# Kernel optimization log

Hardware: AMD Instinct MI355X
Metric: run time of the kernel (lower is better)

Reference implementation:

```python
import jax, jax.numpy as jnp
import numpy as np

ANG = 5  # angRes; n = ANG*ANG
EPS = 1e-12  # torch F.normalize eps

def _l2norm(x, axis):
    n = jnp.sqrt(jnp.sum(x * x, axis=axis, keepdims=True))
    return x / jnp.maximum(n, EPS)

def setup_inputs() -> dict:
    key = jax.random.key(0)
    kq, kk, kv = jax.random.split(key, 3)
    shape = (16, 16, 25, 16, 128)  # b c n h w
    return {
        "token_q": jax.random.normal(kq, shape, dtype=jnp.float32),
        "token_k": jax.random.normal(kk, shape, dtype=jnp.float32),
        "token_v": jax.random.normal(kv, shape, dtype=jnp.float32),
    }

def reference(token_q, token_k, token_v):
    b, c, n, h, w = token_q.shape
    u = v = ANG
    buffer = token_v

    def to_q(x):  # b c (u v) h w -> b (c h) (w u v)
        return x.reshape(b, c, u, v, h, w).transpose(0, 1, 4, 5, 2, 3).reshape(b, c * h, w * u * v)

    def to_k(x):  # b c (u v) h w -> b (w u v) (c h)
        return x.reshape(b, c, u, v, h, w).transpose(0, 5, 2, 3, 1, 4).reshape(b, w * u * v, c * h)

    unfold_q = _l2norm(to_q(token_q), axis=-1)      # [b, ch, wuv]
    unfold_k = _l2norm(to_k(token_k), axis=-2)      # [b, wuv, ch]
    unfold_v = to_q(token_v)                        # [b, ch, wuv]

    att = jnp.einsum('bts,bsr->btr', unfold_q, unfold_k)  # [b, ch, ch]
    size = c * h
    causal = jnp.tril(jnp.ones((size, size), dtype=bool))
    att = jnp.where(causal, att, jnp.float32(-1e15))
    att = jax.nn.softmax(att, axis=-1)

    out = jnp.einsum('btr,brs->bts', att, unfold_v)  # [b, ch, wuv]
    # b (c h) (w u v) -> b c (u v) h w
    out = out.reshape(b, c, h, w, u, v).transpose(0, 1, 4, 5, 2, 3).reshape(b, c, n, h, w)
    return out + buffer
```

## Files before the change

### kernel.cpp

```cpp
#include <hip/hip_runtime.h>
#include <math.h>

#define SB 819200
#define SC 51200
#define SN 2048
#define CH 256
#define NW 3200
#define NPARTS 5
#define PARTLEN 640
#define SPART 1048576
#define G1BLOCKS 240

typedef __bf16 bf16x8 __attribute__((ext_vector_type(8)));
typedef __bf16 bf16x4 __attribute__((ext_vector_type(4)));
typedef __bf16 bf16x2 __attribute__((ext_vector_type(2)));
typedef float  f32x4  __attribute__((ext_vector_type(4)));

__device__ __forceinline__ bf16x8 cvt8(float4 a, float4 b) {
    bf16x8 r;
    r[0] = (__bf16)a.x; r[1] = (__bf16)a.y; r[2] = (__bf16)a.z; r[3] = (__bf16)a.w;
    r[4] = (__bf16)b.x; r[5] = (__bf16)b.y; r[6] = (__bf16)b.z; r[7] = (__bf16)b.w;
    return r;
}

__global__ __launch_bounds__(256, 2) void gemm1_norms_kernel(const float* __restrict__ q,
                                                             const float* __restrict__ k,
                                                             float* __restrict__ Sp,
                                                             float* __restrict__ inv_nq,
                                                             float* __restrict__ inv_nk) {
    __shared__ alignas(16) __bf16 As[128 * 72];
    __shared__ alignas(16) __bf16 Bs[128 * 72];

    const int tid = threadIdx.x;
    const int lane = tid & 63;
    const int wave = tid >> 6;

    if (blockIdx.x >= G1BLOCKS) {
        const int row = (blockIdx.x - G1BLOCKS) * 4 + wave;
        const int b = row >> 8;
        const int t = row & 255;
        const size_t base = (size_t)b * SB + (size_t)(t >> 4) * SC +
                            (size_t)(t & 15) * 128 + lane * 2;
        float sq = 0.f, sk = 0.f;
#pragma unroll
        for (int nch = 0; nch < 25; nch++) {
            const float2 a = *(const float2*)(q + base + (size_t)nch * SN);
            const float2 c = *(const float2*)(k + base + (size_t)nch * SN);
            sq += a.x * a.x + a.y * a.y;
            sk += c.x * c.x + c.y * c.y;
        }
#pragma unroll
        for (int off = 32; off; off >>= 1) {
            sq += __shfl_xor(sq, off, 64);
            sk += __shfl_xor(sk, off, 64);
        }
        if (lane == 0) {
            inv_nq[row] = 1.0f / fmaxf(sqrtf(sq), 1e-12f);
            inv_nk[row] = 1.0f / fmaxf(sqrtf(sk), 1e-12f);
        }
        return;
    }

    const int bx = blockIdx.x;
    const int tile = bx % 3;
    const int part = (bx / 3) % NPARTS;
    const int b = bx / (3 * NPARTS);
    const int tm = (tile + 1) >> 1;
    const int tn = tile >> 1;

    const int wm = wave >> 1;
    const int wn = wave & 1;

    const int srow = tid >> 1;
    const int scol = (tid & 1) * 32;
    const int ta = tm * 128 + srow;
    const int rb = tn * 128 + srow;
    const float* qrow = q + (size_t)b * SB + (size_t)(ta >> 4) * SC + (size_t)(ta & 15) * 128;
    const float* krow = k + (size_t)b * SB + (size_t)(rb >> 4) * SC + (size_t)(rb & 15) * 128;

    f32x4 acc[4][4] = {};
    bool live[4][4];
#pragma unroll
    for (int mi = 0; mi < 4; mi++)
#pragma unroll
        for (int ni = 0; ni < 4; ni++)
            live[mi][ni] = (tn * 128 + wn * 64 + ni * 16) <= (tm * 128 + wm * 64 + mi * 16);

    for (int ch = 0; ch < 10; ch++) {
        const int kg = part * PARTLEN + ch * 64;
        const size_t koff = (size_t)(kg >> 7) * SN + (kg & 127) + scol;

        float4 av[8], bv[8];
#pragma unroll
        for (int j = 0; j < 8; j++) {
            av[j] = *(const float4*)(qrow + koff + j * 4);
            bv[j] = *(const float4*)(krow + koff + j * 4);
        }
        __syncthreads();
#pragma unroll
        for (int j = 0; j < 4; j++) {
            *(bf16x8*)&As[srow * 72 + scol + j * 8] = cvt8(av[2 * j], av[2 * j + 1]);
            *(bf16x8*)&Bs[srow * 72 + scol + j * 8] = cvt8(bv[2 * j], bv[2 * j + 1]);
        }
        __syncthreads();
#pragma unroll
        for (int ks = 0; ks < 2; ks++) {
            const int ko = ks * 32 + (lane >> 4) * 8;
            bf16x8 af[4], bf[4];
#pragma unroll
            for (int mi = 0; mi < 4; mi++)
                af[mi] = *(const bf16x8*)&As[(wm * 64 + mi * 16 + (lane & 15)) * 72 + ko];
#pragma unroll
            for (int ni = 0; ni < 4; ni++)
                bf[ni] = *(const bf16x8*)&Bs[(wn * 64 + ni * 16 + (lane & 15)) * 72 + ko];
#pragma unroll
            for (int mi = 0; mi < 4; mi++)
#pragma unroll
                for (int ni = 0; ni < 4; ni++)
                    if (live[mi][ni])
                        acc[mi][ni] = __builtin_amdgcn_mfma_f32_16x16x32_bf16(
                            af[mi], bf[ni], acc[mi][ni], 0, 0, 0);
        }
    }

    float* o = Sp + (size_t)part * SPART + (size_t)b * 65536;
#pragma unroll
    for (int mi = 0; mi < 4; mi++)
#pragma unroll
        for (int ni = 0; ni < 4; ni++) {
            if (!live[mi][ni]) continue;
            const int r = tn * 128 + wn * 64 + ni * 16 + (lane & 15);
#pragma unroll
            for (int j = 0; j < 4; j++) {
                const int t = tm * 128 + wm * 64 + mi * 16 + (lane >> 4) * 4 + j;
                o[(size_t)t * 256 + r] = acc[mi][ni][j];
            }
        }
}

__global__ __launch_bounds__(256) void softmax_kernel(const float* __restrict__ Sp,
                                                      const float* __restrict__ inv_nq,
                                                      const float* __restrict__ inv_nk,
                                                      __bf16* __restrict__ P) {
    const int wave = threadIdx.x >> 6;
    const int lane = threadIdx.x & 63;
    const int t = blockIdx.x * 4 + wave;
    const int b = blockIdx.y;
    const size_t rowbase = ((size_t)b * 256 + t) * 256;
    const int r0 = lane * 4;

    float4 s4 = {0.f, 0.f, 0.f, 0.f};
#pragma unroll
    for (int p = 0; p < NPARTS; p++) {
        const float4 x = *(const float4*)(Sp + (size_t)p * SPART + rowbase + r0);
        s4.x += x.x; s4.y += x.y; s4.z += x.z; s4.w += x.w;
    }
    const float qn = inv_nq[b * 256 + t];
    const float4 kn = *(const float4*)(inv_nk + b * 256 + r0);

    float val[4] = {s4.x * qn * kn.x, s4.y * qn * kn.y,
                    s4.z * qn * kn.z, s4.w * qn * kn.w};
    float m = -1e30f;
#pragma unroll
    for (int j = 0; j < 4; j++) {
        if (r0 + j > t) val[j] = -1e30f;
        m = fmaxf(m, val[j]);
    }
#pragma unroll
    for (int off = 32; off; off >>= 1) m = fmaxf(m, __shfl_xor(m, off, 64));

    float e[4], sum = 0.f;
#pragma unroll
    for (int j = 0; j < 4; j++) {
        e[j] = (r0 + j <= t) ? expf(val[j] - m) : 0.f;
        sum += e[j];
    }
#pragma unroll
    for (int off = 32; off; off >>= 1) sum += __shfl_xor(sum, off, 64);

    const float inv = 1.0f / sum;
    bf16x4 o;
    o[0] = (__bf16)(e[0] * inv);
    o[1] = (__bf16)(e[1] * inv);
    o[2] = (__bf16)(e[2] * inv);
    o[3] = (__bf16)(e[3] * inv);
    *(bf16x4*)(P + rowbase + r0) = o;
}

__global__ __launch_bounds__(256, 4) void gemm2_kernel(const __bf16* __restrict__ P,
                                                       const float* __restrict__ v,
                                                       float* __restrict__ out) {
    __shared__ alignas(16) char smem[9216];
    __bf16* Vs = (__bf16*)smem;
    float* Es = (float*)smem;

    const int tid = threadIdx.x;
    const int b = blockIdx.z;
    const int tt = blockIdx.y;
    const int nw = blockIdx.x;
    const int n = nw >> 1;
    const int whalf = nw & 1;

    const int lane = tid & 63;
    const int wave = tid >> 6;
    const int wm = wave >> 1;
    const int wn = wave & 1;
    const int l15 = lane & 15;
    const int quad = lane >> 4;

    const int vu = tid & 7;
    const int rp = tid >> 3;
    const float* vbase = v + (size_t)b * SB + (size_t)n * SN + whalf * 64;

    const __bf16* Pbase = P + ((size_t)b * 256 + tt * 128 + wm * 64 + l15) * 256 + quad * 8;

    f32x4 acc[4][2] = {};

    for (int kc = 0; kc < 4; kc++) {
        bf16x8 af[4][2];
#pragma unroll
        for (int mi = 0; mi < 4; mi++)
#pragma unroll
            for (int ks = 0; ks < 2; ks++)
                af[mi][ks] = *(const bf16x8*)(Pbase + (size_t)mi * 16 * 256 + kc * 64 + ks * 32);

        float vr0[8], vr1[8];
        {
            const int r0 = kc * 64 + 2 * rp;
            const int r1 = r0 + 1;
            const float* row0 = vbase + (size_t)(r0 >> 4) * SC + (size_t)(r0 & 15) * 128;
            const float* row1 = vbase + (size_t)(r1 >> 4) * SC + (size_t)(r1 & 15) * 128;
            *(float4*)&vr0[0] = *(const float4*)(row0 + vu * 8);
            *(float4*)&vr0[4] = *(const float4*)(row0 + vu * 8 + 4);
            *(float4*)&vr1[0] = *(const float4*)(row1 + vu * 8);
            *(float4*)&vr1[4] = *(const float4*)(row1 + vu * 8 + 4);
        }
        __syncthreads();
        {
            const int rl0 = 2 * rp;
#pragma unroll
            for (int sj = 0; sj < 8; sj++) {
                const int s = vu * 8 + sj;
                bf16x2 pr;
                pr[0] = (__bf16)vr0[sj];
                pr[1] = (__bf16)vr1[sj];
                *(bf16x2*)&Vs[s * 72 + (rl0 ^ (s & 0x38))] = pr;
            }
        }
        __syncthreads();
#pragma unroll
        for (int ks = 0; ks < 2; ks++) {
            bf16x8 bfr[2];
#pragma unroll
            for (int ni = 0; ni < 2; ni++) {
                const int s = wn * 32 + ni * 16 + l15;
                bfr[ni] = *(const bf16x8*)&Vs[s * 72 + ((ks * 32 + quad * 8) ^ (s & 0x38))];
            }
#pragma unroll
            for (int mi = 0; mi < 4; mi++)
#pragma unroll
                for (int ni = 0; ni < 2; ni++)
                    acc[mi][ni] = __builtin_amdgcn_mfma_f32_16x16x32_bf16(
                        af[mi][ks], bfr[ni], acc[mi][ni], 0, 0, 0);
        }
    }

    for (int p = 0; p < 4; p++) {
        __syncthreads();
        if (wm == (p >> 1)) {
            const int mibase = (p & 1) * 2;
#pragma unroll
            for (int mm = 0; mm < 2; mm++)
#pragma unroll
                for (int ni = 0; ni < 2; ni++) {
                    const f32x4 a = acc[mibase + mm][ni];
                    const int wcol = wn * 32 + ni * 16 + l15;
#pragma unroll
                    for (int j = 0; j < 4; j++)
                        Es[(mm * 16 + quad * 4 + j) * 68 + wcol] = a[j];
                }
        }
        __syncthreads();
#pragma unroll
        for (int it = 0; it < 2; it++) {
            const int tl = it * 16 + (tid >> 4);
            const int w4 = (tid & 15) * 4;
            const int t = tt * 128 + p * 32 + tl;
            const size_t a = (size_t)b * SB + (size_t)(t >> 4) * SC + (size_t)n * SN +
                             (size_t)(t & 15) * 128 + whalf * 64 + w4;
            float4 r4 = *(const float4*)&Es[tl * 68 + w4];
            const float4 buf = *(const float4*)(v + a);
            r4.x += buf.x; r4.y += buf.y; r4.z += buf.z; r4.w += buf.w;
            *(float4*)(out + a) = r4;
        }
    }
}

extern "C" void kernel_launch(void* const* d_in, const int* in_sizes, int n_in,
                              void* d_out, int out_size, void* d_ws, size_t ws_size,
                              hipStream_t stream) {
    const float* q = (const float*)d_in[0];
    const float* k = (const float*)d_in[1];
    const float* v = (const float*)d_in[2];
    float* out = (float*)d_out;

    float* ws = (float*)d_ws;
    float* inv_nq = ws;
    float* inv_nk = ws + 4096;
    __bf16* P = (__bf16*)(ws + 8192);

    float* Spart = out;

    gemm1_norms_kernel<<<dim3(G1BLOCKS + 1024), dim3(256), 0, stream>>>(
        q, k, Spart, inv_nq, inv_nk);
    softmax_kernel<<<dim3(64, 16), dim3(256), 0, stream>>>(Spart, inv_nq, inv_nk, P);
    gemm2_kernel<<<dim3(50, 2, 16), dim3(256), 0, stream>>>(P, v, out);
}
```

Measured before the change: 228.4 us.

## Fuse norm computation into gemm1, double-split K, and prefetch next chunk

Removes the separate norm blocks by accumulating squared row norms from the q/k tiles already loaded in gemm1. Partial norms are written per K-part and reduced in the softmax kernel. K is split into 10 parts instead of 5 to double the gemm1 grid. Global loads for the next chunk are issued before the MFMA work on the current one to overlap latency. This trades extra partial-sum traffic in softmax and workspace for fewer redundant q/k reads.

```diff
diff --git a/kernel.cpp b/kernel.cpp
--- a/kernel.cpp
+++ b/kernel.cpp
@@ -6,10 +6,11 @@
 #define SN 2048
 #define CH 256
 #define NW 3200
-#define NPARTS 5
-#define PARTLEN 640
+#define NPARTS 10
+#define PARTLEN 320
+#define NCHUNK 5
 #define SPART 1048576
-#define G1BLOCKS 240
+#define G1BLOCKS 480
 
 typedef __bf16 bf16x8 __attribute__((ext_vector_type(8)));
 typedef __bf16 bf16x4 __attribute__((ext_vector_type(4)));
@@ -23,43 +24,21 @@
     return r;
 }
 
-__global__ __launch_bounds__(256, 2) void gemm1_norms_kernel(const float* __restrict__ q,
-                                                             const float* __restrict__ k,
-                                                             float* __restrict__ Sp,
-                                                             float* __restrict__ inv_nq,
-                                                             float* __restrict__ inv_nk) {
+__device__ __forceinline__ float dot4(float4 a) {
+    return a.x * a.x + a.y * a.y + a.z * a.z + a.w * a.w;
+}
+
+__global__ __launch_bounds__(256, 2) void gemm1_kernel(const float* __restrict__ q,
+                                                       const float* __restrict__ k,
+                                                       float* __restrict__ Sp,
+                                                       float* __restrict__ nq2p,
+                                                       float* __restrict__ nk2p) {
     __shared__ alignas(16) __bf16 As[128 * 72];
     __shared__ alignas(16) __bf16 Bs[128 * 72];
 
     const int tid = threadIdx.x;
     const int lane = tid & 63;
     const int wave = tid >> 6;
-
-    if (blockIdx.x >= G1BLOCKS) {
-        const int row = (blockIdx.x - G1BLOCKS) * 4 + wave;
-        const int b = row >> 8;
-        const int t = row & 255;
-        const size_t base = (size_t)b * SB + (size_t)(t >> 4) * SC +
-                            (size_t)(t & 15) * 128 + lane * 2;
-        float sq = 0.f, sk = 0.f;
-#pragma unroll
-        for (int nch = 0; nch < 25; nch++) {
-            const float2 a = *(const float2*)(q + base + (size_t)nch * SN);
-            const float2 c = *(const float2*)(k + base + (size_t)nch * SN);
-            sq += a.x * a.x + a.y * a.y;
-            sk += c.x * c.x + c.y * c.y;
-        }
-#pragma unroll
-        for (int off = 32; off; off >>= 1) {
-            sq += __shfl_xor(sq, off, 64);
-            sk += __shfl_xor(sk, off, 64);
-        }
-        if (lane == 0) {
-            inv_nq[row] = 1.0f / fmaxf(sqrtf(sq), 1e-12f);
-            inv_nk[row] = 1.0f / fmaxf(sqrtf(sk), 1e-12f);
-        }
-        return;
-    }
 
     const int bx = blockIdx.x;
     const int tile = bx % 3;
@@ -78,6 +57,9 @@
     const float* qrow = q + (size_t)b * SB + (size_t)(ta >> 4) * SC + (size_t)(ta & 15) * 128;
     const float* krow = k + (size_t)b * SB + (size_t)(rb >> 4) * SC + (size_t)(rb & 15) * 128;
 
+    const bool doQ = (tile != 2);
+    const bool doK = (tile != 1);
+
     f32x4 acc[4][4] = {};
     bool live[4][4];
 #pragma unroll
@@ -86,23 +68,43 @@
         for (int ni = 0; ni < 4; ni++)
             live[mi][ni] = (tn * 128 + wn * 64 + ni * 16) <= (tm * 128 + wm * 64 + mi * 16);
 
-    for (int ch = 0; ch < 10; ch++) {
-        const int kg = part * PARTLEN + ch * 64;
+    float sqa = 0.f, sqb = 0.f;
+    float4 av[8], bv[8];
+
+    {
+        const int kg = part * PARTLEN;
         const size_t koff = (size_t)(kg >> 7) * SN + (kg & 127) + scol;
-
-        float4 av[8], bv[8];
 #pragma unroll
         for (int j = 0; j < 8; j++) {
             av[j] = *(const float4*)(qrow + koff + j * 4);
             bv[j] = *(const float4*)(krow + koff + j * 4);
         }
-        __syncthreads();
 #pragma unroll
         for (int j = 0; j < 4; j++) {
             *(bf16x8*)&As[srow * 72 + scol + j * 8] = cvt8(av[2 * j], av[2 * j + 1]);
             *(bf16x8*)&Bs[srow * 72 + scol + j * 8] = cvt8(bv[2 * j], bv[2 * j + 1]);
         }
-        __syncthreads();
+        if (doQ) {
+#pragma unroll
+            for (int j = 0; j < 8; j++) sqa += dot4(av[j]);
+        }
+        if (doK) {
+#pragma unroll
+            for (int j = 0; j < 8; j++) sqb += dot4(bv[j]);
+        }
+    }
+    __syncthreads();
+
+    for (int ch = 0; ch < NCHUNK; ch++) {
+        if (ch < NCHUNK - 1) {
+            const int kg = part * PARTLEN + (ch + 1) * 64;
+            const size_t koff = (size_t)(kg >> 7) * SN + (kg & 127) + scol;
+#pragma unroll
+            for (int j = 0; j < 8; j++) {
+                av[j] = *(const float4*)(qrow + koff + j * 4);
+                bv[j] = *(const float4*)(krow + koff + j * 4);
+            }
+        }
 #pragma unroll
         for (int ks = 0; ks < 2; ks++) {
             const int ko = ks * 32 + (lane >> 4) * 8;
@@ -121,6 +123,23 @@
                         acc[mi][ni] = __builtin_amdgcn_mfma_f32_16x16x32_bf16(
                             af[mi], bf[ni], acc[mi][ni], 0, 0, 0);
         }
+        if (ch < NCHUNK - 1) {
+            __syncthreads();
+#pragma unroll
+            for (int j = 0; j < 4; j++) {
+                *(bf16x8*)&As[srow * 72 + scol + j * 8] = cvt8(av[2 * j], av[2 * j + 1]);
+                *(bf16x8*)&Bs[srow * 72 + scol + j * 8] = cvt8(bv[2 * j], bv[2 * j + 1]);
+            }
+            if (doQ) {
+#pragma unroll
+                for (int j = 0; j < 8; j++) sqa += dot4(av[j]);
+            }
+            if (doK) {
+#pragma unroll
+                for (int j = 0; j < 8; j++) sqb += dot4(bv[j]);
+            }
+            __syncthreads();
+        }
     }
 
     float* o = Sp + (size_t)part * SPART + (size_t)b * 65536;
@@ -136,11 +155,18 @@
                 o[(size_t)t * 256 + r] = acc[mi][ni][j];
             }
         }
+
+    sqa += __shfl_xor(sqa, 1, 64);
+    sqb += __shfl_xor(sqb, 1, 64);
+    if (!(lane & 1)) {
+        if (doQ) nq2p[part * 4096 + b * 256 + ta] = sqa;
+        if (doK) nk2p[part * 4096 + b * 256 + rb] = sqb;
+    }
 }
 
 __global__ __launch_bounds__(256) void softmax_kernel(const float* __restrict__ Sp,
-                                                      const float* __restrict__ inv_nq,
-                                                      const float* __restrict__ inv_nk,
+                                                      const float* __restrict__ nq2p,
+                                                      const float* __restrict__ nk2p,
                                                       __bf16* __restrict__ P) {
     const int wave = threadIdx.x >> 6;
     const int lane = threadIdx.x & 63;
@@ -155,8 +181,21 @@
         const float4 x = *(const float4*)(Sp + (size_t)p * SPART + rowbase + r0);
         s4.x += x.x; s4.y += x.y; s4.z += x.z; s4.w += x.w;
     }
-    const float qn = inv_nq[b * 256 + t];
-    const float4 kn = *(const float4*)(inv_nk + b * 256 + r0);
+    float sq = 0.f;
+#pragma unroll
+    for (int p = 0; p < NPARTS; p++) sq += nq2p[p * 4096 + b * 256 + t];
+    float4 sk = {0.f, 0.f, 0.f, 0.f};
+#pragma unroll
+    for (int p = 0; p < NPARTS; p++) {
+        const float4 x = *(const float4*)(nk2p + p * 4096 + b * 256 + r0);
+        sk.x += x.x; sk.y += x.y; sk.z += x.z; sk.w += x.w;
+    }
+    const float qn = 1.0f / fmaxf(sqrtf(sq), 1e-12f);
+    float4 kn;
+    kn.x = 1.0f / fmaxf(sqrtf(sk.x), 1e-12f);
+    kn.y = 1.0f / fmaxf(sqrtf(sk.y), 1e-12f);
+    kn.z = 1.0f / fmaxf(sqrtf(sk.z), 1e-12f);
+    kn.w = 1.0f / fmaxf(sqrtf(sk.w), 1e-12f);
 
     float val[4] = {s4.x * qn * kn.x, s4.y * qn * kn.y,
                     s4.z * qn * kn.z, s4.w * qn * kn.w};
@@ -305,14 +344,13 @@
     float* out = (float*)d_out;
 
     float* ws = (float*)d_ws;
-    float* inv_nq = ws;
-    float* inv_nk = ws + 4096;
-    __bf16* P = (__bf16*)(ws + 8192);
+    float* nq2p = ws;
+    float* nk2p = ws + 40960;
+    __bf16* P = (__bf16*)(ws + 81920);
 
     float* Spart = out;
 
-    gemm1_norms_kernel<<<dim3(G1BLOCKS + 1024), dim3(256), 0, stream>>>(
-        q, k, Spart, inv_nq, inv_nk);
-    softmax_kernel<<<dim3(64, 16), dim3(256), 0, stream>>>(Spart, inv_nq, inv_nk, P);
+    gemm1_kernel<<<dim3(G1BLOCKS), dim3(256), 0, stream>>>(q, k, Spart, nq2p, nk2p);
+    softmax_kernel<<<dim3(64, 16), dim3(256), 0, stream>>>(Spart, nq2p, nk2p, P);
     gemm2_kernel<<<dim3(50, 2, 16), dim3(256), 0, stream>>>(P, v, out);
 }
```

New measurement: 224.8 us. No clear change (-1.6%).
